# Kernel tuning notes

Hardware: AMD Instinct MI355X
Metric: run time of the kernel (lower is better)

## Reference

```python
import jax, jax.numpy as jnp
import numpy as np
import math

PHI = (1 + math.sqrt(5)) / 2
PI = math.pi
B, N, T, D, H = 2, 16, 512, 512, 8
DH = D // H
HALF = DH // 2
FF = int(D * PHI)  # 828
DC = D
PR_EPS = 1e-8
LN_EPS = 1e-5


def _ln(x, g, b):
    # x: (B,N,T,D); g,b: (N,D)
    mu = x.mean(axis=-1, keepdims=True)
    var = ((x - mu) ** 2).mean(axis=-1, keepdims=True)
    return (x - mu) * jax.lax.rsqrt(var + LN_EPS) * g[None, :, None, :] + b[None, :, None, :]


def _phase_resonance(a, b):
    # a, b: (B, N, D) in fp32; adjacent feature pairs = (re, im)
    pairs = a.shape[-1] // 2
    def to_phase(x):
        x2 = x.reshape(*x.shape[:-1], pairs, 2)
        return jnp.arctan2(x2[..., 1] + PR_EPS, x2[..., 0] + PR_EPS)
    ta, tb = to_phase(a), to_phase(b)
    delta = ta[..., :, None, :] - tb[..., None, :, :]  # (B, N, N, pairs)
    return jnp.cos(delta).mean(axis=-1)                # (B, N, N) in [-1, 1]


def setup_inputs():
    key = jax.random.key(0)
    ks = iter(jax.random.split(key, 24))
    w = lambda shape: jax.random.normal(next(ks), shape, jnp.float32) * 0.02
    return {
        'x': jax.random.normal(next(ks), (B, N, T, D), jnp.float32),
        'gate_w': w((N, D)),
        'gate_b': jnp.full((N,), 2.0, jnp.float32),  # torch init: bias=2.0
        'ln1_g': jnp.ones((N, D), jnp.float32),
        'ln1_b': jnp.zeros((N, D), jnp.float32),
        'wq': w((N, D, D)), 'wk': w((N, D, D)), 'wv': w((N, D, D)), 'wo': w((N, D, D)),
        'phase_angles': jnp.tile(jnp.linspace(0.0, PI, H, dtype=jnp.float32), (N, 1)),
        'ln2_g': jnp.ones((N, D), jnp.float32),
        'ln2_b': jnp.zeros((N, D), jnp.float32),
        'up_w': w((N, D, FF)), 'up_b': jnp.zeros((N, FF), jnp.float32),
        'down_w': w((N, FF, D)), 'down_b': jnp.zeros((N, D), jnp.float32),
        'commit_w': w((N, D)), 'commit_b': jnp.zeros((N,), jnp.float32),
        'center_w': w((N, D, DC)), 'center_b': jnp.zeros((N, DC), jnp.float32),
        'field_in_w': w((D, D)),
        'field_out_w': w((D, D)),
        'conductance': jnp.float32(1.0),
    }


def reference(x, gate_w, gate_b, ln1_g, ln1_b, wq, wk, wv, wo, phase_angles,
              ln2_g, ln2_b, up_w, up_b, down_w, down_b, commit_w, commit_b,
              center_w, center_b, field_in_w, field_out_w, conductance):
    # ---- BinaryAperture (straight-through binary gate) ----
    logits = jnp.einsum('bntd,nd->bnt', x, gate_w) + gate_b[None, :, None]
    prob = jax.nn.sigmoid(logits)  # temperature = 1.0
    hard = (prob > 0.5).astype(x.dtype)
    gate = (hard + prob - jax.lax.stop_gradient(prob))[..., None]  # (B,N,T,1)

    # ---- Field: phase-rotated, gated attention (scores forced to fp32) ----
    h = _ln(x, ln1_g, ln1_b)
    def proj(wm):
        z = jnp.einsum('bntd,nde->bnte', h, wm)
        return z.reshape(B, N, T, H, DH).transpose(0, 1, 3, 2, 4)  # (B,N,H,T,DH)
    Q, K, V = proj(wq), proj(wk), proj(wv)
    cos_a = jnp.cos(phase_angles)[None, :, :, None, None]  # (1,N,H,1,1)
    sin_a = jnp.sin(phase_angles)[None, :, :, None, None]
    def rot(Z):
        re, im = Z[..., :HALF], Z[..., HALF:2 * HALF]
        return jnp.concatenate([re * cos_a - im * sin_a, re * sin_a + im * cos_a], axis=-1)
    Q, K = rot(Q), rot(K)
    ge = gate[:, :, None]  # (B,N,1,T,1) broadcast over heads
    Q = Q * ge
    K = K * ge
    scores = jnp.einsum('bnhtd,bnhsd->bnhts', Q.astype(jnp.float32), K.astype(jnp.float32)) / math.sqrt(DH)
    attn = jax.nn.softmax(scores, axis=-1).astype(V.dtype)
    field = jnp.einsum('bnhts,bnhsd->bnhtd', attn, V)
    field = field.transpose(0, 1, 3, 2, 4).reshape(B, N, T, D)
    field = jnp.einsum('bntd,nde->bnte', field, wo) * gate
    x = x + field

    # ---- Boundary: golden-ratio FFN gated by commit * gate ----
    h2 = _ln(x, ln2_g, ln2_b)
    up = jax.nn.gelu(jnp.einsum('bntd,ndf->bntf', h2, up_w) + up_b[None, :, None], approximate=False)
    ff = jnp.einsum('bntf,nfd->bntd', up, down_w) + down_b[None, :, None]
    center_pool = x.mean(axis=2)  # (B,N,D) (pooled pre-FFN, as in torch)
    commit = jax.nn.sigmoid(jnp.einsum('bnd,nd->bn', center_pool, commit_w) + commit_b[None])  # (B,N)
    x = x + commit[..., None, None] * gate * ff
    center = jnp.tanh(jnp.einsum('bnd,nde->bne', center_pool, center_w) + center_b[None])  # (B,N,DC)

    # ---- SharedField: phase-resonance coupling across the N nodes ----
    node_gates = commit[..., None]  # (B,N,1)
    transmitted = center * node_gates
    h_res = jnp.einsum('bnd,de->bne', center, field_in_w).astype(jnp.float32)
    r_acc = _phase_resonance(h_res, h_res)  # (B,N,N); r_acc None -> r_acc_new = r_instant
    h_tx = jnp.einsum('bnd,de->bne', transmitted, field_in_w)
    recv = conductance * jnp.einsum('bmn,bnd->bmd', r_acc.astype(x.dtype), h_tx)
    field_signal = jnp.einsum('bnd,de->bne', recv, field_out_w)  # (B,N,D)

    # each node's boundary receives the field signal
    return x + field_signal[:, :, None, :]
```

## Files before the change

### kernel.cpp

```cpp
#include <hip/hip_runtime.h>

typedef unsigned short u16;
typedef __attribute__((ext_vector_type(8))) short short8;
typedef __attribute__((ext_vector_type(4))) float f32x4;

#define B_ 2
#define N_ 16
#define T_ 512
#define D_ 512
#define H_ 8
#define DH_ 64
#define HALF_ 32
#define FF_ 828
#define DC_ 512
#define LN_EPS 1e-5f
#define PR_EPS 1e-8f
#define NEG_INF (-3.0e38f)

__device__ __forceinline__ float b2f(u16 u) { return __uint_as_float(((unsigned)u) << 16); }
__device__ __forceinline__ u16 f2b(float f) {
  unsigned x = __float_as_uint(f);
  return (u16)((x + 0x7fffu + ((x >> 16) & 1u)) >> 16);
}
__device__ __forceinline__ float gelu_exact(float z) {
  return 0.5f * z * (1.f + erff(z * 0.70710678118654752f));
}

__global__ __launch_bounds__(256) void ln_gate_kernel(
    const float* __restrict__ xsrc,
    const float* __restrict__ gate_w, const float* __restrict__ gate_b,
    const float* __restrict__ lng, const float* __restrict__ lnb,
    float* __restrict__ gate_out, u16* __restrict__ h_out, int do_gate) {
  __shared__ float red[256];
  int bnt = blockIdx.x;
  int n = (bnt / T_) % N_;
  int tid = threadIdx.x;
  const float* xr = xsrc + (size_t)bnt * D_;
  float x0 = xr[tid], x1 = xr[tid + 256];
  red[tid] = x0 + x1; __syncthreads();
  for (int s = 128; s > 0; s >>= 1) { if (tid < s) red[tid] += red[tid + s]; __syncthreads(); }
  float mu = red[0] * (1.f / D_); __syncthreads();
  float d0 = x0 - mu, d1 = x1 - mu;
  red[tid] = d0 * d0 + d1 * d1; __syncthreads();
  for (int s = 128; s > 0; s >>= 1) { if (tid < s) red[tid] += red[tid + s]; __syncthreads(); }
  float rstd = rsqrtf(red[0] * (1.f / D_) + LN_EPS); __syncthreads();
  if (do_gate) {
    red[tid] = x0 * gate_w[n * D_ + tid] + x1 * gate_w[n * D_ + tid + 256];
    __syncthreads();
    for (int s = 128; s > 0; s >>= 1) { if (tid < s) red[tid] += red[tid + s]; __syncthreads(); }
    if (tid == 0) gate_out[bnt] = (red[0] + gate_b[n] > 0.f) ? 1.f : 0.f;
  }
  size_t o = (size_t)bnt * D_;
  h_out[o + tid]       = f2b(d0 * rstd * lng[n * D_ + tid]       + lnb[n * D_ + tid]);
  h_out[o + tid + 256] = f2b(d1 * rstd * lng[n * D_ + tid + 256] + lnb[n * D_ + tid + 256]);
}

__global__ __launch_bounds__(256) void wconv_kernel(
    const float* __restrict__ W, u16* __restrict__ Wt, int Kd, int E) {
  __shared__ u16 tile[32][33];
  int e0 = blockIdx.x * 32, k0 = blockIdx.y * 32, n = blockIdx.z;
  const float* Wb = W + (size_t)n * Kd * E;
  u16* Wtb = Wt + (size_t)n * E * Kd;
  int r = threadIdx.x >> 3, c4 = (threadIdx.x & 7) * 4;
  int kk = k0 + r;
  if (kk < Kd) {
    if (e0 + c4 + 3 < E) {
      float4 w4 = *(const float4*)(Wb + (size_t)kk * E + e0 + c4);
      tile[r][c4 + 0] = f2b(w4.x); tile[r][c4 + 1] = f2b(w4.y);
      tile[r][c4 + 2] = f2b(w4.z); tile[r][c4 + 3] = f2b(w4.w);
    } else {
      #pragma unroll
      for (int j = 0; j < 4; ++j) {
        int ee = e0 + c4 + j;
        tile[r][c4 + j] = (ee < E) ? f2b(Wb[(size_t)kk * E + ee]) : (u16)0;
      }
    }
  } else {
    #pragma unroll
    for (int j = 0; j < 4; ++j) tile[r][c4 + j] = 0;
  }
  __syncthreads();
  int ee = e0 + r;
  if (ee < E) {
    u16* dst = Wtb + (size_t)ee * Kd + k0 + c4;
    if (k0 + c4 + 3 < Kd) {
      ushort4 o;
      o.x = tile[c4 + 0][r]; o.y = tile[c4 + 1][r];
      o.z = tile[c4 + 2][r]; o.w = tile[c4 + 3][r];
      *(ushort4*)dst = o;
    } else {
      #pragma unroll
      for (int j = 0; j < 4; ++j) if (k0 + c4 + j < Kd) dst[j] = tile[c4 + j][r];
    }
  }
}

#define BM 128
#define BN 128
#define BK 32
#define LST 40
__global__ __launch_bounds__(256) void gemm_mfma_kernel(
    const u16* __restrict__ In,
    const float* __restrict__ W0, const float* __restrict__ W1, const float* __restrict__ W2,
    const u16* __restrict__ Wt0, const u16* __restrict__ Wt1, const u16* __restrict__ Wt2,
    u16* __restrict__ O0, u16* __restrict__ O1, u16* __restrict__ O2,
    float* __restrict__ OutF,
    int Kd, int E, int mode,
    const float* __restrict__ bias,
    const float* __restrict__ xres, const float* __restrict__ gate) {
  __shared__ u16 As[BM * LST];
  __shared__ u16 Bs[BN * LST];
  int z = blockIdx.z;
  int bn = z & 31, proj = z >> 5;
  int n = bn & (N_ - 1);
  const float* W = (proj == 0) ? W0 : ((proj == 1) ? W1 : W2);
  const u16* Wt = (proj == 0) ? Wt0 : ((proj == 1) ? Wt1 : Wt2);
  u16* Out = (proj == 0) ? O0 : ((proj == 1) ? O1 : O2);
  int e0 = blockIdx.x * BN, t0 = blockIdx.y * BM;
  int tid = threadIdx.x;
  int lane = tid & 63, wave = tid >> 6;
  int m_off = (wave & 1) * 64, n_off = (wave >> 1) * 64;
  int ml = lane & 15, quad = lane >> 4;
  const u16* Inb = In + (size_t)bn * T_ * Kd;
  const float* Wb = W ? W + (size_t)n * Kd * E : nullptr;
  const u16* Wtb = Wt ? Wt + (size_t)n * E * Kd : nullptr;

  f32x4 acc[4][4] = {};

  int ksteps = (Kd + BK - 1) / BK;
  for (int ks = 0; ks < ksteps; ++ks) {
    int k0 = ks * BK;
    #pragma unroll
    for (int it = 0; it < 2; ++it) {
      int slot = tid * 2 + it;
      int r = slot >> 2;
      int q = slot & 3;
      int kg = k0 + q * 8;
      const u16* src = Inb + (size_t)(t0 + r) * Kd + kg;
      u16* dst = &As[r * LST + q * 8];
      if (kg + 8 <= Kd) {
        *(ushort4*)(dst)     = *(const ushort4*)(src);
        *(ushort4*)(dst + 4) = *(const ushort4*)(src + 4);
      } else {
        #pragma unroll
        for (int xx = 0; xx < 8; ++xx) dst[xx] = (kg + xx < Kd) ? src[xx] : (u16)0;
      }
    }
    if (Wtb) {
      #pragma unroll
      for (int it = 0; it < 2; ++it) {
        int slot = tid * 2 + it;
        int r = slot >> 2;
        int q = slot & 3;
        int kg = k0 + q * 8;
        const u16* src = Wtb + (size_t)(e0 + r) * Kd + kg;
        u16* dst = &Bs[r * LST + q * 8];
        if (kg + 8 <= Kd) {
          *(ushort4*)(dst)     = *(const ushort4*)(src);
          *(ushort4*)(dst + 4) = *(const ushort4*)(src + 4);
        } else {
          #pragma unroll
          for (int xx = 0; xx < 8; ++xx) dst[xx] = (kg + xx < Kd) ? src[xx] : (u16)0;
        }
      }
    } else {
      int kk = tid & 31;
      int eb = (tid >> 5) * 16;
      int kg = k0 + kk;
      #pragma unroll
      for (int it = 0; it < 4; ++it) {
        int e = eb + it * 4;
        int eg = e0 + e;
        float4 w4 = {0.f, 0.f, 0.f, 0.f};
        if (kg < Kd && eg < E) w4 = *(const float4*)(Wb + (size_t)kg * E + eg);
        Bs[(e + 0) * LST + kk] = f2b(w4.x);
        Bs[(e + 1) * LST + kk] = f2b(w4.y);
        Bs[(e + 2) * LST + kk] = f2b(w4.z);
        Bs[(e + 3) * LST + kk] = f2b(w4.w);
      }
    }
    __syncthreads();
    short8 a[4], b[4];
    #pragma unroll
    for (int i = 0; i < 4; ++i)
      a[i] = *(const short8*)&As[(m_off + i * 16 + ml) * LST + quad * 8];
    #pragma unroll
    for (int j = 0; j < 4; ++j)
      b[j] = *(const short8*)&Bs[(n_off + j * 16 + ml) * LST + quad * 8];
    #pragma unroll
    for (int i = 0; i < 4; ++i)
      #pragma unroll
      for (int j = 0; j < 4; ++j)
        acc[i][j] = __builtin_amdgcn_mfma_f32_16x16x32_bf16(a[i], b[j], acc[i][j], 0, 0, 0);
    __syncthreads();
  }

  #pragma unroll
  for (int j = 0; j < 4; ++j) {
    int eg = e0 + n_off + j * 16 + ml;
    if (eg >= E) continue;
    #pragma unroll
    for (int i = 0; i < 4; ++i) {
      #pragma unroll
      for (int r = 0; r < 4; ++r) {
        int tg = t0 + m_off + i * 16 + quad * 4 + r;
        float v = acc[i][j][r];
        size_t o = (size_t)bn * T_ * E + (size_t)tg * E + eg;
        if (mode == 0) {
          Out[o] = f2b(v);
        } else if (mode == 1) {
          float g = gate[(size_t)bn * T_ + tg];
          OutF[o] = xres[o] + v * g;
        } else if (mode == 2) {
          Out[o] = f2b(gelu_exact(v + bias[(size_t)n * E + eg]));
        } else {
          Out[o] = f2b(v + bias[(size_t)n * E + eg]);
        }
      }
    }
  }
}

__global__ __launch_bounds__(256) void rot_gate_kernel(
    u16* __restrict__ q, u16* __restrict__ k,
    const float* __restrict__ phase, const float* __restrict__ gate) {
  long long i = (long long)blockIdx.x * 256 + threadIdx.x;
  int c = (int)(i & 31);
  int h = (int)((i >> 5) & 7);
  int t = (int)((i >> 8) & 511);
  int bn = (int)(i >> 17);
  int n = bn & (N_ - 1);
  float a = phase[n * H_ + h];
  float ca = cosf(a), sa = sinf(a);
  float g = gate[(size_t)bn * T_ + t];
  size_t base = ((size_t)bn * T_ + t) * D_ + h * DH_;
  float qr = b2f(q[base + c]), qi = b2f(q[base + c + HALF_]);
  q[base + c]         = f2b((qr * ca - qi * sa) * g);
  q[base + c + HALF_] = f2b((qr * sa + qi * ca) * g);
  float kr = b2f(k[base + c]), ki = b2f(k[base + c + HALF_]);
  k[base + c]         = f2b((kr * ca - ki * sa) * g);
  k[base + c + HALF_] = f2b((kr * sa + ki * ca) * g);
}

#define ATS 72
__global__ __launch_bounds__(256) void attn_kernel(
    const u16* __restrict__ Q, const u16* __restrict__ K, const u16* __restrict__ V,
    u16* __restrict__ O) {
  __shared__ __align__(16) u16 Qs[64 * ATS];
  __shared__ __align__(16) u16 Ks[64 * ATS];
  __shared__ __align__(16) u16 Vs[64 * ATS];
  __shared__ __align__(16) u16 Ps[64 * ATS];
  int qt = blockIdx.x, h = blockIdx.y, bn = blockIdx.z;
  int tid = threadIdx.x;
  int lane = tid & 63, wave = tid >> 6;
  int ml = lane & 15, quad = lane >> 4;
  int t0 = qt * 64;
  size_t rowbase = (size_t)bn * T_ * D_ + (size_t)h * DH_;

  {
    int r = tid >> 2;
    int c = (tid & 3) * 16;
    const u16* src = Q + rowbase + (size_t)(t0 + r) * D_ + c;
    #pragma unroll
    for (int hf = 0; hf < 2; ++hf) {
      short8 v = *(const short8*)(src + hf * 8);
      #pragma unroll
      for (int e = 0; e < 8; ++e)
        ((u16*)&v)[e] = f2b(b2f(((u16*)&v)[e]) * 0.125f);
      *(short8*)&Qs[r * ATS + c + hf * 8] = v;
    }
  }

  float m_[4], l_[4];
  f32x4 acco[4] = {};
  #pragma unroll
  for (int r = 0; r < 4; ++r) { m_[r] = NEG_INF; l_[r] = 0.f; }

  for (int sc = 0; sc < 8; ++sc) {
    int s0 = sc * 64;
    {
      int r = tid >> 2;
      int c = (tid & 3) * 16;
      const u16* src = K + rowbase + (size_t)(s0 + r) * D_ + c;
      *(short8*)&Ks[r * ATS + c]     = *(const short8*)(src);
      *(short8*)&Ks[r * ATS + c + 8] = *(const short8*)(src + 8);
    }
    {
      int sw = wave * 16;
      const u16* src = V + rowbase + (size_t)(s0 + sw) * D_ + lane;
      short8 v0, v1;
      #pragma unroll
      for (int r = 0; r < 8; ++r) ((u16*)&v0)[r] = src[(size_t)r * D_];
      #pragma unroll
      for (int r = 0; r < 8; ++r) ((u16*)&v1)[r] = src[(size_t)(r + 8) * D_];
      *(short8*)&Vs[lane * ATS + sw]     = v0;
      *(short8*)&Vs[lane * ATS + sw + 8] = v1;
    }
    __syncthreads();

    f32x4 s4[4] = {};
    #pragma unroll
    for (int kst = 0; kst < 2; ++kst) {
      short8 a = *(const short8*)&Qs[(wave * 16 + ml) * ATS + kst * 32 + quad * 8];
      #pragma unroll
      for (int j = 0; j < 4; ++j) {
        short8 b = *(const short8*)&Ks[(j * 16 + ml) * ATS + kst * 32 + quad * 8];
        s4[j] = __builtin_amdgcn_mfma_f32_16x16x32_bf16(a, b, s4[j], 0, 0, 0);
      }
    }

    #pragma unroll
    for (int r = 0; r < 4; ++r) {
      float cm = fmaxf(fmaxf(s4[0][r], s4[1][r]), fmaxf(s4[2][r], s4[3][r]));
      #pragma unroll
      for (int off = 1; off < 16; off <<= 1) cm = fmaxf(cm, __shfl_xor(cm, off));
      float mn = fmaxf(m_[r], cm);
      float al = expf(m_[r] - mn);
      u16 q0 = f2b(expf(s4[0][r] - mn)), q1 = f2b(expf(s4[1][r] - mn));
      u16 q2 = f2b(expf(s4[2][r] - mn)), q3 = f2b(expf(s4[3][r] - mn));
      float rs = b2f(q0) + b2f(q1) + b2f(q2) + b2f(q3);
      #pragma unroll
      for (int off = 1; off < 16; off <<= 1) rs += __shfl_xor(rs, off);
      l_[r] = l_[r] * al + rs;
      m_[r] = mn;
      #pragma unroll
      for (int jd = 0; jd < 4; ++jd) acco[jd][r] *= al;
      int trow = wave * 16 + quad * 4 + r;
      Ps[trow * ATS + 0 * 16 + ml] = q0;
      Ps[trow * ATS + 1 * 16 + ml] = q1;
      Ps[trow * ATS + 2 * 16 + ml] = q2;
      Ps[trow * ATS + 3 * 16 + ml] = q3;
    }

    #pragma unroll
    for (int sst = 0; sst < 2; ++sst) {
      short8 a = *(const short8*)&Ps[(wave * 16 + ml) * ATS + sst * 32 + quad * 8];
      #pragma unroll
      for (int jd = 0; jd < 4; ++jd) {
        short8 b = *(const short8*)&Vs[(jd * 16 + ml) * ATS + sst * 32 + quad * 8];
        acco[jd] = __builtin_amdgcn_mfma_f32_16x16x32_bf16(a, b, acco[jd], 0, 0, 0);
      }
    }
    __syncthreads();
  }

  #pragma unroll
  for (int r = 0; r < 4; ++r) {
    float inv = 1.f / l_[r];
    int trow = t0 + wave * 16 + quad * 4 + r;
    #pragma unroll
    for (int jd = 0; jd < 4; ++jd)
      O[rowbase + (size_t)trow * D_ + jd * 16 + ml] = f2b(acco[jd][r] * inv);
  }
}

__global__ __launch_bounds__(256) void pool_kernel(const float* __restrict__ x2, float* __restrict__ cp) {
  int bid = blockIdx.x;
  int bn = bid >> 1;
  int d = (bid & 1) * 256 + threadIdx.x;
  const float* base = x2 + (size_t)bn * T_ * D_ + d;
  float s = 0.f;
  for (int t = 0; t < T_; ++t) s += base[(size_t)t * D_];
  cp[(size_t)bn * D_ + d] = s * (1.f / T_);
}

__global__ __launch_bounds__(256) void commit_center_kernel(
    const float* __restrict__ cp, const float* __restrict__ commit_w, const float* __restrict__ commit_b,
    const float* __restrict__ center_w, const float* __restrict__ center_b,
    float* __restrict__ commit, float* __restrict__ center) {
  __shared__ float cps[512];
  __shared__ float red[256];
  int bn = blockIdx.x, n = bn % N_, tid = threadIdx.x;
  cps[tid] = cp[(size_t)bn * D_ + tid];
  cps[tid + 256] = cp[(size_t)bn * D_ + tid + 256];
  __syncthreads();
  red[tid] = cps[tid] * commit_w[n * D_ + tid] + cps[tid + 256] * commit_w[n * D_ + tid + 256];
  __syncthreads();
  for (int s = 128; s > 0; s >>= 1) { if (tid < s) red[tid] += red[tid + s]; __syncthreads(); }
  if (tid == 0) commit[bn] = 1.f / (1.f + expf(-(red[0] + commit_b[n])));
  #pragma unroll
  for (int eo = 0; eo < 2; ++eo) {
    int e = eo * 256 + tid;
    float acc = center_b[(size_t)n * DC_ + e];
    for (int d = 0; d < D_; ++d) acc = fmaf(cps[d], center_w[((size_t)n * D_ + d) * DC_ + e], acc);
    center[(size_t)bn * DC_ + e] = tanhf(acc);
  }
}

__global__ __launch_bounds__(256) void matvec_kernel(
    const float* __restrict__ inp, const float* __restrict__ Wm, float* __restrict__ outp) {
  __shared__ float s[512];
  int bn = blockIdx.x, tid = threadIdx.x;
  s[tid] = inp[(size_t)bn * D_ + tid];
  s[tid + 256] = inp[(size_t)bn * D_ + tid + 256];
  __syncthreads();
  #pragma unroll
  for (int eo = 0; eo < 2; ++eo) {
    int e = eo * 256 + tid;
    float acc = 0.f;
    for (int d = 0; d < D_; ++d) acc = fmaf(s[d], Wm[(size_t)d * D_ + e], acc);
    outp[(size_t)bn * D_ + e] = acc;
  }
}

__global__ __launch_bounds__(256) void uv_kernel(
    const float* __restrict__ hres, float* __restrict__ u, float* __restrict__ v) {
  int i = blockIdx.x * 256 + threadIdx.x;
  float xr = hres[2 * i] + PR_EPS;
  float yi = hres[2 * i + 1] + PR_EPS;
  float r = sqrtf(xr * xr + yi * yi);
  u[i] = xr / r; v[i] = yi / r;
}

__global__ __launch_bounds__(256) void racc_kernel(
    const float* __restrict__ u, const float* __restrict__ v, float* __restrict__ ra) {
  int b = blockIdx.x, tid = threadIdx.x;
  int mm = tid >> 4, nn = tid & 15;
  const float* ub = u + (size_t)b * N_ * 256;
  const float* vb = v + (size_t)b * N_ * 256;
  float acc = 0.f;
  for (int p = 0; p < 256; ++p)
    acc += ub[mm * 256 + p] * ub[nn * 256 + p] + vb[mm * 256 + p] * vb[nn * 256 + p];
  ra[(size_t)b * N_ * N_ + mm * N_ + nn] = acc * (1.f / 256.f);
}

__global__ __launch_bounds__(256) void recv_kernel(
    const float* __restrict__ ra, const float* __restrict__ commit,
    const float* __restrict__ hres, const float* __restrict__ cond, float* __restrict__ recv) {
  int bn = blockIdx.x, b = bn / N_, mm = bn % N_, tid = threadIdx.x;
  float c = cond[0];
  #pragma unroll
  for (int eo = 0; eo < 2; ++eo) {
    int d = eo * 256 + tid;
    float acc = 0.f;
    for (int nn = 0; nn < N_; ++nn)
      acc += ra[(size_t)b * N_ * N_ + mm * N_ + nn] * commit[b * N_ + nn] *
             hres[((size_t)b * N_ + nn) * D_ + d];
    recv[(size_t)bn * D_ + d] = c * acc;
  }
}

__global__ __launch_bounds__(256) void final_kernel(
    const float* __restrict__ x2, const float* __restrict__ commit,
    const float* __restrict__ gate, const u16* __restrict__ ff,
    const float* __restrict__ fs, float* __restrict__ out) {
  long long i4 = (long long)blockIdx.x * 256 + threadIdx.x;
  long long base = i4 * 4;
  int d = (int)(base & (D_ - 1));
  int t = (int)((base >> 9) & (T_ - 1));
  int bn = (int)(base >> 18);
  float cg = commit[bn] * gate[(size_t)bn * T_ + t];
  float4 xv = *(const float4*)(x2 + base);
  ushort4 fv = *(const ushort4*)(ff + base);
  float4 sv = *(const float4*)(fs + (size_t)bn * D_ + d);
  float4 r;
  r.x = xv.x + cg * b2f(fv.x) + sv.x;
  r.y = xv.y + cg * b2f(fv.y) + sv.y;
  r.z = xv.z + cg * b2f(fv.z) + sv.z;
  r.w = xv.w + cg * b2f(fv.w) + sv.w;
  *(float4*)(out + base) = r;
}

extern "C" void kernel_launch(void* const* d_in, const int* in_sizes, int n_in,
                              void* d_out, int out_size, void* d_ws, size_t ws_size,
                              hipStream_t stream) {
  (void)in_sizes; (void)n_in; (void)out_size;
  const float* x          = (const float*)d_in[0];
  const float* gate_w     = (const float*)d_in[1];
  const float* gate_b     = (const float*)d_in[2];
  const float* ln1_g      = (const float*)d_in[3];
  const float* ln1_b      = (const float*)d_in[4];
  const float* wq         = (const float*)d_in[5];
  const float* wk         = (const float*)d_in[6];
  const float* wv         = (const float*)d_in[7];
  const float* wo         = (const float*)d_in[8];
  const float* phase      = (const float*)d_in[9];
  const float* ln2_g      = (const float*)d_in[10];
  const float* ln2_b      = (const float*)d_in[11];
  const float* up_w       = (const float*)d_in[12];
  const float* up_b       = (const float*)d_in[13];
  const float* down_w     = (const float*)d_in[14];
  const float* down_b     = (const float*)d_in[15];
  const float* commit_w   = (const float*)d_in[16];
  const float* commit_b   = (const float*)d_in[17];
  const float* center_w   = (const float*)d_in[18];
  const float* center_b   = (const float*)d_in[19];
  const float* field_in_w = (const float*)d_in[20];
  const float* field_out_w= (const float*)d_in[21];
  const float* cond       = (const float*)d_in[22];

  const long long BNTD = 8388608LL;
  u16* w16 = (u16*)d_ws;
  u16* R0 = w16;
  u16* R1 = w16 + BNTD;
  u16* R2 = w16 + 2 * BNTD;
  u16* R3 = w16 + 3 * BNTD;
  float* sm   = (float*)(w16 + 4 * BNTD);
  float* gate   = sm;
  float* cp     = sm + 16384;
  float* center = sm + 2 * 16384;
  float* hres   = sm + 3 * 16384;
  float* uu     = sm + 4 * 16384;
  float* vv     = uu + 8192;
  float* ra     = vv + 8192;
  float* recvb  = ra + 512;
  float* fsig   = recvb + 16384;
  float* commit = fsig + 16384;
  float* x2 = (float*)d_out;

  const size_t WSQ = (size_t)N_ * 512 * 512;
  const size_t WUP = (size_t)N_ * 512 * 828;
  u16* wtbase = (u16*)(sm + 115232);
  u16* wtq = wtbase;
  u16* wtk = wtq + WSQ;
  u16* wtv = wtk + WSQ;
  u16* wto = wtv + WSQ;
  u16* wtu = wto + WSQ;
  u16* wtd = wtu + WUP;
  size_t needed = (size_t)((char*)(wtd + WUP) - (char*)d_ws);
  bool use_wt = ws_size >= needed;

  ln_gate_kernel<<<16384, 256, 0, stream>>>(x, gate_w, gate_b, ln1_g, ln1_b, gate, R0, 1);

  if (use_wt) {
    wconv_kernel<<<dim3(16, 16, 16), 256, 0, stream>>>(wq, wtq, 512, 512);
    wconv_kernel<<<dim3(16, 16, 16), 256, 0, stream>>>(wk, wtk, 512, 512);
    wconv_kernel<<<dim3(16, 16, 16), 256, 0, stream>>>(wv, wtv, 512, 512);
    wconv_kernel<<<dim3(16, 16, 16), 256, 0, stream>>>(wo, wto, 512, 512);
    wconv_kernel<<<dim3(26, 16, 16), 256, 0, stream>>>(up_w, wtu, 512, 828);
    wconv_kernel<<<dim3(16, 26, 16), 256, 0, stream>>>(down_w, wtd, 828, 512);
  }
  const u16* pq = use_wt ? wtq : nullptr;
  const u16* pk = use_wt ? wtk : nullptr;
  const u16* pv = use_wt ? wtv : nullptr;
  const u16* po = use_wt ? wto : nullptr;
  const u16* pu = use_wt ? wtu : nullptr;
  const u16* pd = use_wt ? wtd : nullptr;

  gemm_mfma_kernel<<<dim3(4, 4, 96), 256, 0, stream>>>(
      R0, wq, wk, wv, pq, pk, pv, R1, R2, R3, nullptr, 512, 512, 0, nullptr, nullptr, nullptr);
  rot_gate_kernel<<<16384, 256, 0, stream>>>(R1, R2, phase, gate);
  attn_kernel<<<dim3(8, 8, 32), 256, 0, stream>>>(R1, R2, R3, R0);
  gemm_mfma_kernel<<<dim3(4, 4, 32), 256, 0, stream>>>(
      R0, wo, nullptr, nullptr, po, nullptr, nullptr, nullptr, nullptr, nullptr, x2,
      512, 512, 1, nullptr, x, gate);
  ln_gate_kernel<<<16384, 256, 0, stream>>>(x2, nullptr, nullptr, ln2_g, ln2_b, nullptr, R1, 0);
  gemm_mfma_kernel<<<dim3(7, 4, 32), 256, 0, stream>>>(
      R1, up_w, nullptr, nullptr, pu, nullptr, nullptr, R2, nullptr, nullptr, nullptr,
      512, 828, 2, up_b, nullptr, nullptr);
  gemm_mfma_kernel<<<dim3(4, 4, 32), 256, 0, stream>>>(
      R2, down_w, nullptr, nullptr, pd, nullptr, nullptr, R0, nullptr, nullptr, nullptr,
      828, 512, 3, down_b, nullptr, nullptr);
  pool_kernel<<<64, 256, 0, stream>>>(x2, cp);
  commit_center_kernel<<<32, 256, 0, stream>>>(cp, commit_w, commit_b, center_w, center_b, commit, center);
  matvec_kernel<<<32, 256, 0, stream>>>(center, field_in_w, hres);
  uv_kernel<<<32, 256, 0, stream>>>(hres, uu, vv);
  racc_kernel<<<2, 256, 0, stream>>>(uu, vv, ra);
  recv_kernel<<<32, 256, 0, stream>>>(ra, commit, hres, cond, recvb);
  matvec_kernel<<<32, 256, 0, stream>>>(recvb, field_out_w, fsig);
  final_kernel<<<8192, 256, 0, stream>>>(x2, commit, gate, R0, fsig, x2);
}
```

Baseline: 886.2 us.

## Use direct global-to-LDS loads with XOR-swizzled LDS and padded FFN dims

The GEMM kernel now fills its A and B shared-memory tiles with global_load_lds DMA instructions instead of going through registers, and replaces padded LDS rows with an XOR swizzle to avoid bank conflicts. The FFN hidden dimension is padded from 828 to 832 so that every K step is aligned and needs no boundary handling. Padded columns are written as zeros. The aim is less register and VALU traffic in the load path, in exchange for tighter layout constraints and extra padding work.

Result: faster. 812.0 us (-8.4%).

```diff
diff --git a/kernel.cpp b/kernel.cpp
--- a/kernel.cpp
+++ b/kernel.cpp
@@ -12,6 +12,7 @@
 #define DH_ 64
 #define HALF_ 32
 #define FF_ 828
+#define FFP_ 832
 #define DC_ 512
 #define LN_EPS 1e-5f
 #define PR_EPS 1e-8f
@@ -24,6 +25,12 @@
 }
 __device__ __forceinline__ float gelu_exact(float z) {
   return 0.5f * z * (1.f + erff(z * 0.70710678118654752f));
+}
+
+typedef __attribute__((address_space(1))) const unsigned GASu;
+typedef __attribute__((address_space(3))) unsigned LASu;
+__device__ __forceinline__ void gload_lds16(const void* g, void* l) {
+  __builtin_amdgcn_global_load_lds((GASu*)g, (LASu*)l, 16, 0, 0);
 }
 
 __global__ __launch_bounds__(256) void ln_gate_kernel(
@@ -56,11 +63,11 @@
 }
 
 __global__ __launch_bounds__(256) void wconv_kernel(
-    const float* __restrict__ W, u16* __restrict__ Wt, int Kd, int E) {
+    const float* __restrict__ W, u16* __restrict__ Wt, int Kd, int E, int Kpad) {
   __shared__ u16 tile[32][33];
   int e0 = blockIdx.x * 32, k0 = blockIdx.y * 32, n = blockIdx.z;
   const float* Wb = W + (size_t)n * Kd * E;
-  u16* Wtb = Wt + (size_t)n * E * Kd;
+  u16* Wtb = Wt + (size_t)n * E * Kpad;
   int r = threadIdx.x >> 3, c4 = (threadIdx.x & 7) * 4;
   int kk = k0 + r;
   if (kk < Kd) {
@@ -82,15 +89,15 @@
   __syncthreads();
   int ee = e0 + r;
   if (ee < E) {
-    u16* dst = Wtb + (size_t)ee * Kd + k0 + c4;
-    if (k0 + c4 + 3 < Kd) {
+    u16* dst = Wtb + (size_t)ee * Kpad + k0 + c4;
+    if (k0 + c4 + 3 < Kpad) {
       ushort4 o;
       o.x = tile[c4 + 0][r]; o.y = tile[c4 + 1][r];
       o.z = tile[c4 + 2][r]; o.w = tile[c4 + 3][r];
       *(ushort4*)dst = o;
     } else {
       #pragma unroll
-      for (int j = 0; j < 4; ++j) if (k0 + c4 + j < Kd) dst[j] = tile[c4 + j][r];
+      for (int j = 0; j < 4; ++j) if (k0 + c4 + j < Kpad) dst[j] = tile[c4 + j][r];
     }
   }
 }
@@ -98,18 +105,17 @@
 #define BM 128
 #define BN 128
 #define BK 32
-#define LST 40
 __global__ __launch_bounds__(256) void gemm_mfma_kernel(
     const u16* __restrict__ In,
     const float* __restrict__ W0, const float* __restrict__ W1, const float* __restrict__ W2,
     const u16* __restrict__ Wt0, const u16* __restrict__ Wt1, const u16* __restrict__ Wt2,
     u16* __restrict__ O0, u16* __restrict__ O1, u16* __restrict__ O2,
     float* __restrict__ OutF,
-    int Kd, int E, int mode,
+    int Kd, int KdW, int E, int Es, int mode,
     const float* __restrict__ bias,
     const float* __restrict__ xres, const float* __restrict__ gate) {
-  __shared__ u16 As[BM * LST];
-  __shared__ u16 Bs[BN * LST];
+  __shared__ __align__(16) u16 As[BM * BK];
+  __shared__ __align__(16) u16 Bs[BN * BK];
   int z = blockIdx.z;
   int bn = z & 31, proj = z >> 5;
   int n = bn & (N_ - 1);
@@ -122,71 +128,67 @@
   int m_off = (wave & 1) * 64, n_off = (wave >> 1) * 64;
   int ml = lane & 15, quad = lane >> 4;
   const u16* Inb = In + (size_t)bn * T_ * Kd;
-  const float* Wb = W ? W + (size_t)n * Kd * E : nullptr;
+  const float* Wb = W ? W + (size_t)n * (size_t)KdW * E : nullptr;
   const u16* Wtb = Wt ? Wt + (size_t)n * E * Kd : nullptr;
+
+  int srow = (wave * 2) * 16 + (lane >> 2);
+  int sg0 = (lane & 3) ^ ((srow >> 1) & 3);
+  int sg1 = (lane & 3) ^ (((srow + 16) >> 1) & 3);
+  int swz = (quad ^ ((ml >> 1) & 3)) * 8;
 
   f32x4 acc[4][4] = {};
 
   int ksteps = (Kd + BK - 1) / BK;
   for (int ks = 0; ks < ksteps; ++ks) {
     int k0 = ks * BK;
-    #pragma unroll
-    for (int it = 0; it < 2; ++it) {
-      int slot = tid * 2 + it;
-      int r = slot >> 2;
-      int q = slot & 3;
-      int kg = k0 + q * 8;
-      const u16* src = Inb + (size_t)(t0 + r) * Kd + kg;
-      u16* dst = &As[r * LST + q * 8];
-      if (kg + 8 <= Kd) {
-        *(ushort4*)(dst)     = *(const ushort4*)(src);
-        *(ushort4*)(dst + 4) = *(const ushort4*)(src + 4);
-      } else {
-        #pragma unroll
-        for (int xx = 0; xx < 8; ++xx) dst[xx] = (kg + xx < Kd) ? src[xx] : (u16)0;
-      }
-    }
     if (Wtb) {
+      int i0 = wave * 2;
+      gload_lds16(Inb + (size_t)(t0 + srow) * Kd + k0 + sg0 * 8, &As[i0 * 512]);
+      gload_lds16(Inb + (size_t)(t0 + srow + 16) * Kd + k0 + sg1 * 8, &As[(i0 + 1) * 512]);
+      gload_lds16(Wtb + (size_t)(e0 + srow) * Kd + k0 + sg0 * 8, &Bs[i0 * 512]);
+      gload_lds16(Wtb + (size_t)(e0 + srow + 16) * Kd + k0 + sg1 * 8, &Bs[(i0 + 1) * 512]);
+    } else {
       #pragma unroll
       for (int it = 0; it < 2; ++it) {
         int slot = tid * 2 + it;
         int r = slot >> 2;
         int q = slot & 3;
         int kg = k0 + q * 8;
-        const u16* src = Wtb + (size_t)(e0 + r) * Kd + kg;
-        u16* dst = &Bs[r * LST + q * 8];
+        const u16* src = Inb + (size_t)(t0 + r) * Kd + kg;
+        u16* dst = &As[r * BK + (q ^ ((r >> 1) & 3)) * 8];
         if (kg + 8 <= Kd) {
-          *(ushort4*)(dst)     = *(const ushort4*)(src);
-          *(ushort4*)(dst + 4) = *(const ushort4*)(src + 4);
+          *(short8*)dst = *(const short8*)src;
         } else {
           #pragma unroll
           for (int xx = 0; xx < 8; ++xx) dst[xx] = (kg + xx < Kd) ? src[xx] : (u16)0;
         }
       }
-    } else {
-      int kk = tid & 31;
-      int eb = (tid >> 5) * 16;
-      int kg = k0 + kk;
-      #pragma unroll
-      for (int it = 0; it < 4; ++it) {
-        int e = eb + it * 4;
-        int eg = e0 + e;
-        float4 w4 = {0.f, 0.f, 0.f, 0.f};
-        if (kg < Kd && eg < E) w4 = *(const float4*)(Wb + (size_t)kg * E + eg);
-        Bs[(e + 0) * LST + kk] = f2b(w4.x);
-        Bs[(e + 1) * LST + kk] = f2b(w4.y);
-        Bs[(e + 2) * LST + kk] = f2b(w4.z);
-        Bs[(e + 3) * LST + kk] = f2b(w4.w);
+      {
+        int kk = tid & 31;
+        int eb = (tid >> 5) * 16;
+        int kg = k0 + kk;
+        int s = kk >> 3, w = kk & 7;
+        #pragma unroll
+        for (int it = 0; it < 4; ++it) {
+          int e = eb + it * 4;
+          int eg = e0 + e;
+          float4 w4 = {0.f, 0.f, 0.f, 0.f};
+          if (kg < KdW && eg < E) w4 = *(const float4*)(Wb + (size_t)kg * E + eg);
+          Bs[(e + 0) * BK + ((s ^ (((e + 0) >> 1) & 3)) * 8) + w] = f2b(w4.x);
+          Bs[(e + 1) * BK + ((s ^ (((e + 1) >> 1) & 3)) * 8) + w] = f2b(w4.y);
+          Bs[(e + 2) * BK + ((s ^ (((e + 2) >> 1) & 3)) * 8) + w] = f2b(w4.z);
+          Bs[(e + 3) * BK + ((s ^ (((e + 3) >> 1) & 3)) * 8) + w] = f2b(w4.w);
+        }
       }
     }
     __syncthreads();
     short8 a[4], b[4];
     #pragma unroll
     for (int i = 0; i < 4; ++i)
-      a[i] = *(const short8*)&As[(m_off + i * 16 + ml) * LST + quad * 8];
+      a[i] = *(const short8*)&As[(m_off + i * 16 + ml) * BK + swz];
     #pragma unroll
     for (int j = 0; j < 4; ++j)
-      b[j] = *(const short8*)&Bs[(n_off + j * 16 + ml) * LST + quad * 8];
+      b[j] = *(const short8*)&Bs[(n_off + j * 16 + ml) * BK + swz];
     #pragma unroll
     for (int i = 0; i < 4; ++i)
       #pragma unroll
@@ -198,21 +200,21 @@
   #pragma unroll
   for (int j = 0; j < 4; ++j) {
     int eg = e0 + n_off + j * 16 + ml;
-    if (eg >= E) continue;
+    if (eg >= Es) continue;
     #pragma unroll
     for (int i = 0; i < 4; ++i) {
       #pragma unroll
       for (int r = 0; r < 4; ++r) {
         int tg = t0 + m_off + i * 16 + quad * 4 + r;
         float v = acc[i][j][r];
-        size_t o = (size_t)bn * T_ * E + (size_t)tg * E + eg;
+        size_t o = (size_t)bn * T_ * Es + (size_t)tg * Es + eg;
         if (mode == 0) {
           Out[o] = f2b(v);
         } else if (mode == 1) {
           float g = gate[(size_t)bn * T_ + tg];
           OutF[o] = xres[o] + v * g;
         } else if (mode == 2) {
-          Out[o] = f2b(gelu_exact(v + bias[(size_t)n * E + eg]));
+          Out[o] = (eg < E) ? f2b(gelu_exact(v + bias[(size_t)n * E + eg])) : (u16)0;
         } else {
           Out[o] = f2b(v + bias[(size_t)n * E + eg]);
         }
@@ -509,26 +511,27 @@
   float* x2 = (float*)d_out;
 
   const size_t WSQ = (size_t)N_ * 512 * 512;
-  const size_t WUP = (size_t)N_ * 512 * 828;
+  const size_t WUPu = (size_t)N_ * 828 * 512;
+  const size_t WUPd = (size_t)N_ * 512 * 832;
   u16* wtbase = (u16*)(sm + 115232);
   u16* wtq = wtbase;
   u16* wtk = wtq + WSQ;
   u16* wtv = wtk + WSQ;
   u16* wto = wtv + WSQ;
   u16* wtu = wto + WSQ;
-  u16* wtd = wtu + WUP;
-  size_t needed = (size_t)((char*)(wtd + WUP) - (char*)d_ws);
+  u16* wtd = wtu + WUPu;
+  size_t needed = (size_t)((char*)(wtd + WUPd) - (char*)d_ws);
   bool use_wt = ws_size >= needed;
 
   ln_gate_kernel<<<16384, 256, 0, stream>>>(x, gate_w, gate_b, ln1_g, ln1_b, gate, R0, 1);
 
   if (use_wt) {
-    wconv_kernel<<<dim3(16, 16, 16), 256, 0, stream>>>(wq, wtq, 512, 512);
-    wconv_kernel<<<dim3(16, 16, 16), 256, 0, stream>>>(wk, wtk, 512, 512);
-    wconv_kernel<<<dim3(16, 16, 16), 256, 0, stream>>>(wv, wtv, 512, 512);
-    wconv_kernel<<<dim3(16, 16, 16), 256, 0, stream>>>(wo, wto, 512, 512);
-    wconv_kernel<<<dim3(26, 16, 16), 256, 0, stream>>>(up_w, wtu, 512, 828);
-    wconv_kernel<<<dim3(16, 26, 16), 256, 0, stream>>>(down_w, wtd, 828, 512);
+    wconv_kernel<<<dim3(16, 16, 16), 256, 0, stream>>>(wq, wtq, 512, 512, 512);
+    wconv_kernel<<<dim3(16, 16, 16), 256, 0, stream>>>(wk, wtk, 512, 512, 512);
+    wconv_kernel<<<dim3(16, 16, 16), 256, 0, stream>>>(wv, wtv, 512, 512, 512);
+    wconv_kernel<<<dim3(16, 16, 16), 256, 0, stream>>>(wo, wto, 512, 512, 512);
+    wconv_kernel<<<dim3(26, 16, 16), 256, 0, stream>>>(up_w, wtu, 512, 828, 512);
+    wconv_kernel<<<dim3(16, 26, 16), 256, 0, stream>>>(down_w, wtd, 828, 512, 832);
   }
   const u16* pq = use_wt ? wtq : nullptr;
   const u16* pk = use_wt ? wtk : nullptr;
@@ -538,19 +541,20 @@
   const u16* pd = use_wt ? wtd : nullptr;
 
   gemm_mfma_kernel<<<dim3(4, 4, 96), 256, 0, stream>>>(
-      R0, wq, wk, wv, pq, pk, pv, R1, R2, R3, nullptr, 512, 512, 0, nullptr, nullptr, nullptr);
+      R0, wq, wk, wv, pq, pk, pv, R1, R2, R3, nullptr,
+      512, 512, 512, 512, 0, nullptr, nullptr, nullptr);
   rot_gate_kernel<<<16384, 256, 0, stream>>>(R1, R2, phase, gate);
   attn_kernel<<<dim3(8, 8, 32), 256, 0, stream>>>(R1, R2, R3, R0);
   gemm_mfma_kernel<<<dim3(4, 4, 32), 256, 0, stream>>>(
       R0, wo, nullptr, nullptr, po, nullptr, nullptr, nullptr, nullptr, nullptr, x2,
-      512, 512, 1, nullptr, x, gate);
+      512, 512, 512, 512, 1, nullptr, x, gate);
   ln_gate_kernel<<<16384, 256, 0, stream>>>(x2, nullptr, nullptr, ln2_g, ln2_b, nullptr, R1, 0);
   gemm_mfma_kernel<<<dim3(7, 4, 32), 256, 0, stream>>>(
       R1, up_w, nullptr, nullptr, pu, nullptr, nullptr, R2, nullptr, nullptr, nullptr,
-      512, 828, 2, up_b, nullptr, nullptr);
+      512, 512, 828, 832, 2, up_b, nullptr, nullptr);
   gemm_mfma_kernel<<<dim3(4, 4, 32), 256, 0, stream>>>(
       R2, down_w, nullptr, nullptr, pd, nullptr, nullptr, R0, nullptr, nullptr, nullptr,
-      828, 512, 3, down_b, nullptr, nullptr);
+      832, 828, 512, 512, 3, down_b, nullptr, nullptr);
   pool_kernel<<<64, 256, 0, stream>>>(x2, cp);
   commit_center_kernel<<<32, 256, 0, stream>>>(cp, commit_w, commit_b, center_w, center_b, commit, center);
   matvec_kernel<<<32, 256, 0, stream>>>(center, field_in_w, hres);
```
